# Kernel tuning notes

Measured on AMD Instinct MI355X. Metric: run time of the kernel, lower is better.

## Reference

```python
import jax, jax.numpy as jnp
import numpy as np

N = 50000      # nodes
E = 500000     # edges (before self-loops)
D_IN = 128     # embedding_dim
C = 256        # intermediate_dim (per-head out channels)
H = 1          # heads
SLOPE = 0.2    # LeakyReLU negative slope (PyG default)


def setup_inputs() -> dict:
    key = jax.random.key(0)
    ks = jax.random.split(key, 8)
    x = jax.random.normal(ks[0], (N, D_IN), dtype=jnp.float32)
    edge_index = jax.random.randint(ks[1], (2, E), 0, N, dtype=jnp.int32)
    W1 = jax.random.normal(ks[2], (H * C, D_IN), dtype=jnp.float32) / np.sqrt(D_IN)
    a1_src = jax.random.normal(ks[3], (H, C), dtype=jnp.float32) / np.sqrt(C)
    a1_dst = jax.random.normal(ks[4], (H, C), dtype=jnp.float32) / np.sqrt(C)
    b1 = jnp.zeros((C,), dtype=jnp.float32)
    W2 = jax.random.normal(ks[5], (H * C, C), dtype=jnp.float32) / np.sqrt(C)
    a2_src = jax.random.normal(ks[6], (H, C), dtype=jnp.float32) / np.sqrt(C)
    a2_dst = jax.random.normal(ks[7], (H, C), dtype=jnp.float32) / np.sqrt(C)
    b2 = jnp.zeros((C,), dtype=jnp.float32)
    return dict(x=x, edge_index=edge_index, W1=W1, a1_src=a1_src, a1_dst=a1_dst,
                b1=b1, W2=W2, a2_src=a2_src, a2_dst=a2_dst, b2=b2)


def gat_conv(x, src, dst, W, a_src, a_dst, b):
    # x: [N, Din]; W: [H*C, Din]; a_*: [H, C]; b: [C]
    h = (x @ W.T).reshape(N, H, C)                      # [N, H, C]
    e_src = jnp.einsum('nhc,hc->nh', h, a_src)          # [N, H]
    e_dst = jnp.einsum('nhc,hc->nh', h, a_dst)          # [N, H]
    e = jax.nn.leaky_relu(e_src[src] + e_dst[dst], SLOPE)  # [Etot, H]
    # segment softmax over destination nodes (self-loops guarantee >=1 edge per node)
    m = jax.lax.stop_gradient(jax.ops.segment_max(e, dst, num_segments=N))
    p = jnp.exp(e - m[dst])                             # [Etot, H]
    denom = jax.ops.segment_sum(p, dst, num_segments=N)  # [N, H]
    alpha = p / (denom[dst] + 1e-16)                    # [Etot, H]
    out = jax.ops.segment_sum(h[src] * alpha[:, :, None], dst, num_segments=N)  # [N, H, C]
    return out.mean(axis=1) + b                         # concat=False -> head mean; [N, C]


def reference(x, edge_index, W1, a1_src, a1_dst, b1, W2, a2_src, a2_dst, b2):
    # PyG GATConv default add_self_loops=True
    loop = jnp.arange(N, dtype=edge_index.dtype)
    src = jnp.concatenate([edge_index[0], loop])
    dst = jnp.concatenate([edge_index[1], loop])
    x1 = jax.nn.relu(gat_conv(x, src, dst, W1, a1_src, a1_dst, b1))
    x2 = jax.nn.relu(gat_conv(x1, src, dst, W2, a2_src, a2_dst, b2))
    return jnp.concatenate([x1, x2], axis=-1)           # [N, 2*C]
```

## Files before the change

### kernel.cpp

```cpp
#include <hip/hip_runtime.h>
#include <hip/hip_bf16.h>
#include <math.h>

#define NNODES 50000
#define NEDGES 500000
#define ETOT   (NEDGES + NNODES)
#define DIN    128
#define CH     256
#define SLOPE  0.2f

#define SCAN_TILE 1024
#define NSCAN ((NNODES + SCAN_TILE - 1) / SCAN_TILE)

typedef __attribute__((ext_vector_type(8))) short short8;
typedef __attribute__((ext_vector_type(4))) float f32x4;

static __device__ __forceinline__ float wave_reduce_max(float v) {
#pragma unroll
  for (int off = 32; off > 0; off >>= 1) v = fmaxf(v, __shfl_xor(v, off));
  return v;
}
static __device__ __forceinline__ float wave_reduce_sum(float v) {
#pragma unroll
  for (int off = 32; off > 0; off >>= 1) v += __shfl_xor(v, off);
  return v;
}

static __device__ __forceinline__ unsigned short f2bf(float f) {
  unsigned int u = __float_as_uint(f);
  unsigned int r = (u + 0x7fffu + ((u >> 16) & 1u)) >> 16;
  return (unsigned short)r;
}
static __device__ __forceinline__ float bf2f(unsigned short u) {
  return __uint_as_float(((unsigned int)u) << 16);
}

__global__ void degree_kernel(const int* __restrict__ ei, int* __restrict__ deg) {
  int e = blockIdx.x * blockDim.x + threadIdx.x;
  if (e >= ETOT) return;
  int dst = (e < NEDGES) ? ei[NEDGES + e] : (e - NEDGES);
  atomicAdd(&deg[dst], 1);
}

__global__ __launch_bounds__(256) void scan_blocksums(const int* __restrict__ deg,
                                                      int* __restrict__ bsums) {
  __shared__ int sdata[4];
  int b = blockIdx.x;
  int tid = threadIdx.x;
  int idx = b * SCAN_TILE + tid * 4;
  int s = 0;
  if (idx + 3 < NNODES) {
    int4 v = *(const int4*)(deg + idx);
    s = v.x + v.y + v.z + v.w;
  } else {
#pragma unroll
    for (int j = 0; j < 4; j++) if (idx + j < NNODES) s += deg[idx + j];
  }
#pragma unroll
  for (int off = 32; off > 0; off >>= 1) s += __shfl_xor(s, off);
  if ((tid & 63) == 0) sdata[tid >> 6] = s;
  __syncthreads();
  if (tid == 0) bsums[b] = sdata[0] + sdata[1] + sdata[2] + sdata[3];
}

__global__ __launch_bounds__(64) void scan_bsums(const int* __restrict__ bsums,
                                                 int* __restrict__ boffs,
                                                 int* __restrict__ rowptr) {
  int tid = threadIdx.x;
  int v = (tid < NSCAN) ? bsums[tid] : 0;
  int x = v;
#pragma unroll
  for (int off = 1; off < 64; off <<= 1) {
    int t = __shfl_up(x, off);
    if (tid >= off) x += t;
  }
  if (tid < NSCAN) boffs[tid] = x - v;
  if (tid == 63) rowptr[NNODES] = x;
}

__global__ __launch_bounds__(256) void scan_final(const int* __restrict__ deg,
                                                  const int* __restrict__ boffs,
                                                  int* __restrict__ rowptr,
                                                  int* __restrict__ cursor) {
  __shared__ int wsums[4];
  int b = blockIdx.x;
  int tid = threadIdx.x;
  int lane = tid & 63;
  int base = b * SCAN_TILE + tid * 4;
  int d[4];
  int s = 0;
#pragma unroll
  for (int j = 0; j < 4; j++) {
    d[j] = (base + j < NNODES) ? deg[base + j] : 0;
    s += d[j];
  }
  int x = s;
#pragma unroll
  for (int off = 1; off < 64; off <<= 1) {
    int t = __shfl_up(x, off);
    if (lane >= off) x += t;
  }
  if (lane == 63) wsums[tid >> 6] = x;
  __syncthreads();
  int woff = 0;
  int w = tid >> 6;
  for (int i = 0; i < w; i++) woff += wsums[i];
  int excl = boffs[b] + woff + (x - s);
#pragma unroll
  for (int j = 0; j < 4; j++) {
    if (base + j < NNODES) { rowptr[base + j] = excl; cursor[base + j] = excl; }
    excl += d[j];
  }
}

__global__ void scatter_kernel(const int* __restrict__ ei, int* __restrict__ cursor,
                               int* __restrict__ csr_src) {
  int e = blockIdx.x * blockDim.x + threadIdx.x;
  if (e >= ETOT) return;
  int src, dst;
  if (e < NEDGES) { src = ei[e]; dst = ei[NEDGES + e]; }
  else            { src = e - NEDGES; dst = src; }
  int slot = atomicAdd(&cursor[dst], 1);
  csr_src[slot] = src;
}

__global__ void cast_f32_bf16(const float* __restrict__ in,
                              unsigned short* __restrict__ outp, int n4) {
  int i = blockIdx.x * blockDim.x + threadIdx.x;
  if (i >= n4) return;
  float4 v = *(const float4*)(in + (size_t)i * 4);
  ushort4 o;
  o.x = f2bf(v.x); o.y = f2bf(v.y); o.z = f2bf(v.z); o.w = f2bf(v.w);
  *(ushort4*)(outp + (size_t)i * 4) = o;
}

#define TM 128
#define TN 128
#define TK 64
#define LDA (TK + 8)

__global__ __launch_bounds__(256) void gemm_bf16(
    const unsigned short* __restrict__ X, int ldx,
    const unsigned short* __restrict__ W, int K,
    unsigned short* __restrict__ Hout, int M) {
  __shared__ short As[TM * LDA];
  __shared__ short Bs[TN * LDA];
  int bm = blockIdx.y * TM;
  int bn = blockIdx.x * TN;
  int tid = threadIdx.x;
  int wid = tid >> 6;
  int lane = tid & 63;
  int wm = (wid & 1) * 64;
  int wn = (wid >> 1) * 64;
  int lrow = lane & 15;
  int lk8 = (lane >> 4) * 8;

  int srow = tid >> 3;
  int skoff = (tid & 7) * 8;

  f32x4 acc[4][4] = {};

  for (int k0 = 0; k0 < K; k0 += TK) {
#pragma unroll
    for (int i = 0; i < 4; i++) {
      int r = srow + 32 * i;
      int gm = bm + r;
      short8 v = {};
      if (gm < M) v = *(const short8*)(X + (size_t)gm * ldx + k0 + skoff);
      *(short8*)(&As[r * LDA + skoff]) = v;
      short8 w = *(const short8*)(W + (size_t)(bn + r) * K + k0 + skoff);
      *(short8*)(&Bs[r * LDA + skoff]) = w;
    }
    __syncthreads();
#pragma unroll
    for (int kk = 0; kk < TK; kk += 32) {
      short8 a[4], b[4];
#pragma unroll
      for (int mi = 0; mi < 4; mi++)
        a[mi] = *(const short8*)(&As[(wm + mi * 16 + lrow) * LDA + kk + lk8]);
#pragma unroll
      for (int ni = 0; ni < 4; ni++)
        b[ni] = *(const short8*)(&Bs[(wn + ni * 16 + lrow) * LDA + kk + lk8]);
#pragma unroll
      for (int mi = 0; mi < 4; mi++)
#pragma unroll
        for (int ni = 0; ni < 4; ni++)
          acc[mi][ni] = __builtin_amdgcn_mfma_f32_16x16x32_bf16(a[mi], b[ni], acc[mi][ni], 0, 0, 0);
    }
    __syncthreads();
  }

  int crow = (lane >> 4) * 4;
  int ccol = lane & 15;
#pragma unroll
  for (int mi = 0; mi < 4; mi++) {
#pragma unroll
    for (int ni = 0; ni < 4; ni++) {
#pragma unroll
      for (int r = 0; r < 4; r++) {
        int gm = bm + wm + mi * 16 + crow + r;
        if (gm < M)
          Hout[(size_t)gm * CH + bn + wn + ni * 16 + ccol] = f2bf(acc[mi][ni][r]);
      }
    }
  }
}

__global__ __launch_bounds__(256) void score_kernel(const unsigned short* __restrict__ Hmb,
                                                    const float* __restrict__ a_src,
                                                    const float* __restrict__ a_dst,
                                                    float* __restrict__ eS,
                                                    float* __restrict__ eD) {
  int n = blockIdx.x * 4 + (threadIdx.x >> 6);
  if (n >= NNODES) return;
  int lane = threadIdx.x & 63;
  ushort4 hu = *(const ushort4*)(Hmb + (size_t)n * CH + lane * 4);
  float4 as = *(const float4*)(a_src + lane * 4);
  float4 ad = *(const float4*)(a_dst + lane * 4);
  float h0 = bf2f(hu.x), h1 = bf2f(hu.y), h2 = bf2f(hu.z), h3 = bf2f(hu.w);
  float s = h0 * as.x + h1 * as.y + h2 * as.z + h3 * as.w;
  float d = h0 * ad.x + h1 * ad.y + h2 * ad.z + h3 * ad.w;
  s = wave_reduce_sum(s);
  d = wave_reduce_sum(d);
  if (lane == 0) { eS[n] = s; eD[n] = d; }
}

__global__ __launch_bounds__(256) void aggregate_kernel(
    const unsigned short* __restrict__ Hmb, const float* __restrict__ eS,
    const float* __restrict__ eD, const int* __restrict__ rowptr,
    const int* __restrict__ csr_src, const float* __restrict__ bias,
    float* __restrict__ out, int outOffset, unsigned short* __restrict__ xout) {
  int n = blockIdx.x * 4 + (threadIdx.x >> 6);
  if (n >= NNODES) return;
  int lane = threadIdx.x & 63;
  int beg = rowptr[n], end = rowptr[n + 1];
  int deg = end - beg;
  float ed = eD[n];

  float4 acc = make_float4(0.f, 0.f, 0.f, 0.f);

  if (deg <= 64) {
    int src = 0;
    float e = -1e30f;
    if (lane < deg) {
      src = csr_src[beg + lane];
      float t = eS[src] + ed;
      e = (t >= 0.f) ? t : SLOPE * t;
    }
    float m = wave_reduce_max(e);
    float p = (lane < deg) ? __expf(e - m) : 0.f;
    float inv = 1.f / (wave_reduce_sum(p) + 1e-16f);

    for (int j0 = 0; j0 < deg; j0 += 4) {
      ushort4 hv[4];
      float al[4];
#pragma unroll
      for (int t = 0; t < 4; t++) {
        int j = j0 + t;
        int jj = (j < deg) ? j : 0;
        int sj = __shfl(src, jj);
        float aj = __shfl(p, jj) * inv;
        al[t] = (j < deg) ? aj : 0.f;
        hv[t] = *(const ushort4*)(Hmb + (size_t)sj * CH + lane * 4);
      }
#pragma unroll
      for (int t = 0; t < 4; t++) {
        acc.x += al[t] * bf2f(hv[t].x);
        acc.y += al[t] * bf2f(hv[t].y);
        acc.z += al[t] * bf2f(hv[t].z);
        acc.w += al[t] * bf2f(hv[t].w);
      }
    }
  } else {
    float m = -1e30f;
    for (int i = lane; i < deg; i += 64) {
      float e = eS[csr_src[beg + i]] + ed;
      e = (e >= 0.f) ? e : SLOPE * e;
      m = fmaxf(m, e);
    }
    m = wave_reduce_max(m);
    float ds = 0.f;
    for (int i = lane; i < deg; i += 64) {
      float e = eS[csr_src[beg + i]] + ed;
      e = (e >= 0.f) ? e : SLOPE * e;
      ds += __expf(e - m);
    }
    ds = wave_reduce_sum(ds) + 1e-16f;
    float inv = 1.f / ds;
    for (int k = beg; k < end; k++) {
      int s = csr_src[k];
      float e = eS[s] + ed;
      e = (e >= 0.f) ? e : SLOPE * e;
      float alpha = __expf(e - m) * inv;
      ushort4 hu = *(const ushort4*)(Hmb + (size_t)s * CH + lane * 4);
      acc.x += alpha * bf2f(hu.x); acc.y += alpha * bf2f(hu.y);
      acc.z += alpha * bf2f(hu.z); acc.w += alpha * bf2f(hu.w);
    }
  }

  float4 b = *(const float4*)(bias + lane * 4);
  float4 o;
  o.x = fmaxf(acc.x + b.x, 0.f);
  o.y = fmaxf(acc.y + b.y, 0.f);
  o.z = fmaxf(acc.z + b.z, 0.f);
  o.w = fmaxf(acc.w + b.w, 0.f);
  *(float4*)(out + (size_t)n * 512 + outOffset + lane * 4) = o;
  if (xout) {
    ushort4 ob;
    ob.x = f2bf(o.x); ob.y = f2bf(o.y); ob.z = f2bf(o.z); ob.w = f2bf(o.w);
    *(ushort4*)(xout + (size_t)n * CH + lane * 4) = ob;
  }
}

extern "C" void kernel_launch(void* const* d_in, const int* in_sizes, int n_in,
                              void* d_out, int out_size, void* d_ws, size_t ws_size,
                              hipStream_t stream) {
  const float* x   = (const float*)d_in[0];
  const int*   ei  = (const int*)d_in[1];
  const float* W1  = (const float*)d_in[2];
  const float* a1s = (const float*)d_in[3];
  const float* a1d = (const float*)d_in[4];
  const float* b1  = (const float*)d_in[5];
  const float* W2  = (const float*)d_in[6];
  const float* a2s = (const float*)d_in[7];
  const float* a2d = (const float*)d_in[8];
  const float* b2  = (const float*)d_in[9];
  float* out = (float*)d_out;

  char* ws = (char*)d_ws;
  size_t off = 0;
  auto alloc = [&](size_t bytes) -> void* {
    void* p = ws + off;
    off = (off + bytes + 255) & ~(size_t)255;
    return p;
  };
  unsigned short* Hmb    = (unsigned short*)alloc(sizeof(short) * (size_t)NNODES * CH);
  unsigned short* Xb     = (unsigned short*)alloc(sizeof(short) * (size_t)NNODES * CH);
  unsigned short* Wb     = (unsigned short*)alloc(sizeof(short) * CH * CH);
  float*          eS     = (float*)alloc(sizeof(float) * NNODES);
  float*          eD     = (float*)alloc(sizeof(float) * NNODES);
  int*            rowptr = (int*)alloc(sizeof(int) * (NNODES + 1));
  int*            cursor = (int*)alloc(sizeof(int) * NNODES);
  int*            csrsrc = (int*)alloc(sizeof(int) * ETOT);
  int*            deg    = (int*)alloc(sizeof(int) * NNODES);
  int*            bsums  = (int*)alloc(sizeof(int) * NSCAN);
  int*            boffs  = (int*)alloc(sizeof(int) * NSCAN);

  hipMemsetAsync(deg, 0, sizeof(int) * NNODES, stream);
  degree_kernel<<<(ETOT + 255) / 256, 256, 0, stream>>>(ei, deg);
  scan_blocksums<<<NSCAN, 256, 0, stream>>>(deg, bsums);
  scan_bsums<<<1, 64, 0, stream>>>(bsums, boffs, rowptr);
  scan_final<<<NSCAN, 256, 0, stream>>>(deg, boffs, rowptr, cursor);
  scatter_kernel<<<(ETOT + 255) / 256, 256, 0, stream>>>(ei, cursor, csrsrc);

  dim3 gemm_grid(2, (NNODES + TM - 1) / TM);
  int nblk4 = (NNODES + 3) / 4;

  {
    int n4 = NNODES * DIN / 4;
    cast_f32_bf16<<<(n4 + 255) / 256, 256, 0, stream>>>(x, Xb, n4);
    int w4 = CH * DIN / 4;
    cast_f32_bf16<<<(w4 + 255) / 256, 256, 0, stream>>>(W1, Wb, w4);
  }
  gemm_bf16<<<gemm_grid, 256, 0, stream>>>(Xb, DIN, Wb, DIN, Hmb, NNODES);
  score_kernel<<<nblk4, 256, 0, stream>>>(Hmb, a1s, a1d, eS, eD);
  aggregate_kernel<<<nblk4, 256, 0, stream>>>(Hmb, eS, eD, rowptr, csrsrc, b1, out, 0, Xb);

  {
    int w4 = CH * CH / 4;
    cast_f32_bf16<<<(w4 + 255) / 256, 256, 0, stream>>>(W2, Wb, w4);
  }
  gemm_bf16<<<gemm_grid, 256, 0, stream>>>(Xb, CH, Wb, CH, Hmb, NNODES);
  score_kernel<<<nblk4, 256, 0, stream>>>(Hmb, a2s, a2d, eS, eD);
  aggregate_kernel<<<nblk4, 256, 0, stream>>>(Hmb, eS, eD, rowptr, csrsrc, b2, out, 256, (unsigned short*)nullptr);
}
```

Baseline: 344.6 us.

## Fuse input cast and attention scores into GEMM, unroll aggregation gather deeper

The fp32-to-bf16 cast of x now happens inside the first GEMM's tile load, and the standalone score kernel is removed. Attention scores are instead computed from the fp32 accumulators in the GEMM epilogue, reduced across lanes, and accumulated with atomics into zeroed buffers. The aggregation loop now gathers 8 neighbour rows per iteration instead of 4, giving more memory-level parallelism. In exchange it adds memsets, atomics (two column blocks per row, so the summation order can vary) and scores computed before bf16 rounding, which differs slightly from the previous path.

```diff
diff --git a/kernel.cpp b/kernel.cpp
--- a/kernel.cpp
+++ b/kernel.cpp
@@ -140,9 +140,11 @@
 #define LDA (TK + 8)
 
 __global__ __launch_bounds__(256) void gemm_bf16(
-    const unsigned short* __restrict__ X, int ldx,
+    const float* __restrict__ Xf, const unsigned short* __restrict__ Xb, int ldx,
     const unsigned short* __restrict__ W, int K,
-    unsigned short* __restrict__ Hout, int M) {
+    unsigned short* __restrict__ Hout, int M,
+    const float* __restrict__ a_src, const float* __restrict__ a_dst,
+    float* __restrict__ eS, float* __restrict__ eD) {
   __shared__ short As[TM * LDA];
   __shared__ short Bs[TN * LDA];
   int bm = blockIdx.y * TM;
@@ -166,7 +168,19 @@
       int r = srow + 32 * i;
       int gm = bm + r;
       short8 v = {};
-      if (gm < M) v = *(const short8*)(X + (size_t)gm * ldx + k0 + skoff);
+      if (gm < M) {
+        if (Xf) {
+          const float* p = Xf + (size_t)gm * ldx + k0 + skoff;
+          float4 f0 = *(const float4*)(p);
+          float4 f1 = *(const float4*)(p + 4);
+          v[0] = (short)f2bf(f0.x); v[1] = (short)f2bf(f0.y);
+          v[2] = (short)f2bf(f0.z); v[3] = (short)f2bf(f0.w);
+          v[4] = (short)f2bf(f1.x); v[5] = (short)f2bf(f1.y);
+          v[6] = (short)f2bf(f1.z); v[7] = (short)f2bf(f1.w);
+        } else {
+          v = *(const short8*)(Xb + (size_t)gm * ldx + k0 + skoff);
+        }
+      }
       *(short8*)(&As[r * LDA + skoff]) = v;
       short8 w = *(const short8*)(W + (size_t)(bn + r) * K + k0 + skoff);
       *(short8*)(&Bs[r * LDA + skoff]) = w;
@@ -192,6 +206,7 @@
 
   int crow = (lane >> 4) * 4;
   int ccol = lane & 15;
+
 #pragma unroll
   for (int mi = 0; mi < 4; mi++) {
 #pragma unroll
@@ -204,25 +219,37 @@
       }
     }
   }
-}
-
-__global__ __launch_bounds__(256) void score_kernel(const unsigned short* __restrict__ Hmb,
-                                                    const float* __restrict__ a_src,
-                                                    const float* __restrict__ a_dst,
-                                                    float* __restrict__ eS,
-                                                    float* __restrict__ eD) {
-  int n = blockIdx.x * 4 + (threadIdx.x >> 6);
-  if (n >= NNODES) return;
-  int lane = threadIdx.x & 63;
-  ushort4 hu = *(const ushort4*)(Hmb + (size_t)n * CH + lane * 4);
-  float4 as = *(const float4*)(a_src + lane * 4);
-  float4 ad = *(const float4*)(a_dst + lane * 4);
-  float h0 = bf2f(hu.x), h1 = bf2f(hu.y), h2 = bf2f(hu.z), h3 = bf2f(hu.w);
-  float s = h0 * as.x + h1 * as.y + h2 * as.z + h3 * as.w;
-  float d = h0 * ad.x + h1 * ad.y + h2 * ad.z + h3 * ad.w;
-  s = wave_reduce_sum(s);
-  d = wave_reduce_sum(d);
-  if (lane == 0) { eS[n] = s; eD[n] = d; }
+
+  float asv[4], adv[4];
+#pragma unroll
+  for (int ni = 0; ni < 4; ni++) {
+    int c = bn + wn + ni * 16 + ccol;
+    asv[ni] = a_src[c];
+    adv[ni] = a_dst[c];
+  }
+#pragma unroll
+  for (int mi = 0; mi < 4; mi++) {
+#pragma unroll
+    for (int r = 0; r < 4; r++) {
+      float s = 0.f, d = 0.f;
+#pragma unroll
+      for (int ni = 0; ni < 4; ni++) {
+        float h = acc[mi][ni][r];
+        s += h * asv[ni];
+        d += h * adv[ni];
+      }
+#pragma unroll
+      for (int off = 1; off < 16; off <<= 1) {
+        s += __shfl_xor(s, off);
+        d += __shfl_xor(d, off);
+      }
+      int gm = bm + wm + mi * 16 + crow + r;
+      if (ccol == 0 && gm < M) {
+        atomicAdd(&eS[gm], s);
+        atomicAdd(&eD[gm], d);
+      }
+    }
+  }
 }
 
 __global__ __launch_bounds__(256) void aggregate_kernel(
@@ -251,20 +278,20 @@
     float p = (lane < deg) ? __expf(e - m) : 0.f;
     float inv = 1.f / (wave_reduce_sum(p) + 1e-16f);
 
-    for (int j0 = 0; j0 < deg; j0 += 4) {
-      ushort4 hv[4];
-      float al[4];
-#pragma unroll
-      for (int t = 0; t < 4; t++) {
+    for (int j0 = 0; j0 < deg; j0 += 8) {
+      ushort4 hv[8];
+      float al[8];
+#pragma unroll
+      for (int t = 0; t < 8; t++) {
         int j = j0 + t;
-        int jj = (j < deg) ? j : 0;
+        int jj = (j < deg) ? j : deg - 1;
         int sj = __shfl(src, jj);
         float aj = __shfl(p, jj) * inv;
         al[t] = (j < deg) ? aj : 0.f;
         hv[t] = *(const ushort4*)(Hmb + (size_t)sj * CH + lane * 4);
       }
 #pragma unroll
-      for (int t = 0; t < 4; t++) {
+      for (int t = 0; t < 8; t++) {
         acc.x += al[t] * bf2f(hv[t].x);
         acc.y += al[t] * bf2f(hv[t].y);
         acc.z += al[t] * bf2f(hv[t].z);
@@ -357,20 +384,22 @@
   int nblk4 = (NNODES + 3) / 4;
 
   {
-    int n4 = NNODES * DIN / 4;
-    cast_f32_bf16<<<(n4 + 255) / 256, 256, 0, stream>>>(x, Xb, n4);
     int w4 = CH * DIN / 4;
     cast_f32_bf16<<<(w4 + 255) / 256, 256, 0, stream>>>(W1, Wb, w4);
   }
-  gemm_bf16<<<gemm_grid, 256, 0, stream>>>(Xb, DIN, Wb, DIN, Hmb, NNODES);
-  score_kernel<<<nblk4, 256, 0, stream>>>(Hmb, a1s, a1d, eS, eD);
+  hipMemsetAsync(eS, 0, sizeof(float) * NNODES, stream);
+  hipMemsetAsync(eD, 0, sizeof(float) * NNODES, stream);
+  gemm_bf16<<<gemm_grid, 256, 0, stream>>>(x, (const unsigned short*)nullptr, DIN,
+                                           Wb, DIN, Hmb, NNODES, a1s, a1d, eS, eD);
   aggregate_kernel<<<nblk4, 256, 0, stream>>>(Hmb, eS, eD, rowptr, csrsrc, b1, out, 0, Xb);
 
   {
     int w4 = CH * CH / 4;
     cast_f32_bf16<<<(w4 + 255) / 256, 256, 0, stream>>>(W2, Wb, w4);
   }
-  gemm_bf16<<<gemm_grid, 256, 0, stream>>>(Xb, CH, Wb, CH, Hmb, NNODES);
-  score_kernel<<<nblk4, 256, 0, stream>>>(Hmb, a2s, a2d, eS, eD);
+  hipMemsetAsync(eS, 0, sizeof(float) * NNODES, stream);
+  hipMemsetAsync(eD, 0, sizeof(float) * NNODES, stream);
+  gemm_bf16<<<gemm_grid, 256, 0, stream>>>((const float*)nullptr, Xb, CH,
+                                           Wb, CH, Hmb, NNODES, a2s, a2d, eS, eD);
   aggregate_kernel<<<nblk4, 256, 0, stream>>>(Hmb, eS, eD, rowptr, csrsrc, b2, out, 256, (unsigned short*)nullptr);
 }
```

Result: no change. 350.8 us (+1.8%).
